# Kernel tuning notes

Measured on AMD Instinct MI355X. Metric: run time of the kernel, lower is better.

Reference implementation:

```python
import jax, jax.numpy as jnp
import numpy as np

D_MODEL = 1024
N_HEADS = 16
D_HEAD = 64
B, S = 2, 2048


def setup_inputs() -> dict:
    key = jax.random.key(0)
    ks = jax.random.split(key, 16)
    HDH = N_HEADS * D_HEAD
    s = 0.02
    return {
        "h": jax.random.normal(ks[0], (B, S, D_MODEL), dtype=jnp.float32),
        "att_mask": jax.random.randint(ks[1], (B, S), 0, 2) > 0,
        "Wq": jax.random.normal(ks[2], (D_MODEL, HDH), dtype=jnp.float32) * s,
        "bq": jnp.zeros((HDH,), dtype=jnp.float32),
        "Wkv": jax.random.normal(ks[3], (D_MODEL, 2 * HDH), dtype=jnp.float32) * s,
        "bkv": jnp.zeros((2 * HDH,), dtype=jnp.float32),
        "Wo": jax.random.normal(ks[4], (HDH, D_MODEL), dtype=jnp.float32) * s,
        "bo": jnp.zeros((D_MODEL,), dtype=jnp.float32),
        "W1": jax.random.normal(ks[5], (D_MODEL, D_MODEL), dtype=jnp.float32) * s,
        "b1": jnp.zeros((D_MODEL,), dtype=jnp.float32),
        "W2": jax.random.normal(ks[6], (D_MODEL, D_MODEL), dtype=jnp.float32) * s,
        "b2": jnp.zeros((D_MODEL,), dtype=jnp.float32),
        "ln_g": jnp.ones((D_MODEL,), dtype=jnp.float32),
        "ln_b": jnp.zeros((D_MODEL,), dtype=jnp.float32),
    }


def _layer_norm(x, g, b, eps=1e-6):
    mu = jnp.mean(x, axis=-1, keepdims=True)
    var = jnp.mean(jnp.square(x - mu), axis=-1, keepdims=True)
    return (x - mu) * jax.lax.rsqrt(var + eps) * g + b


def reference(h, att_mask, Wq, bq, Wkv, bkv, Wo, bo, W1, b1, W2, b2, ln_g, ln_b):
    bz, ln, _ = h.shape
    scale = 1.0 / (D_HEAD ** 0.5)
    q = (h @ Wq + bq).reshape(bz, ln, N_HEADS, D_HEAD)
    kv = h @ Wkv + bkv
    k, v = jnp.split(kv, 2, axis=-1)
    k = k.reshape(bz, ln, N_HEADS, D_HEAD)
    v = v.reshape(bz, ln, N_HEADS, D_HEAD)
    # scores: [b, heads, len_q, len_k]
    scores = jnp.einsum('bqhd,bkhd->bhqk', q, k) * scale
    scores = jnp.where(att_mask[:, None, None, :], -1e9, scores)
    probs = jax.nn.softmax(scores, axis=-1)
    att = jnp.einsum('bhqk,bkhd->bqhd', probs, v).reshape(bz, ln, N_HEADS * D_HEAD)
    att_out = att @ Wo + bo
    # glu_type == 1
    g = jax.nn.sigmoid(h @ W1 + b1) * (h @ W2 + b2)
    return _layer_norm(h + att_out + g, ln_g, ln_b)
```

## Files before the change

kernel.cpp:

```cpp
#include <hip/hip_runtime.h>
#include <hip/hip_bf16.h>


typedef short bf16x8 __attribute__((ext_vector_type(8)));
typedef float f32x4  __attribute__((ext_vector_type(4)));
typedef float f32x16 __attribute__((ext_vector_type(16)));
typedef unsigned int u32x4 __attribute__((ext_vector_type(4)));

typedef const __attribute__((address_space(1))) void* gas_cvp;
typedef __attribute__((address_space(3))) void* las_vp;

__device__ __forceinline__ void gload_lds16(const void* g, void* l) {
  __builtin_amdgcn_global_load_lds((gas_cvp)g, (las_vp)l, 16, 0, 0);
}

__device__ __forceinline__ short f2bf(float f) {
  __hip_bfloat16 h = __float2bfloat16(f);
  return *reinterpret_cast<short*>(&h);
}
__device__ __forceinline__ float bf2f(short s) {
  unsigned u = ((unsigned)(unsigned short)s) << 16;
  return __builtin_bit_cast(float, u);
}

#if __has_builtin(__builtin_amdgcn_exp2f)
#define EXP2(x) __builtin_amdgcn_exp2f(x)
#else
#define EXP2(x) exp2f(x)
#endif

constexpr int BATCH = 2;
constexpr int SEQ   = 2048;
constexpr int NH    = 16;
constexpr int MROWS = BATCH * SEQ;
constexpr int NSPLIT = 2;
constexpr int KSPL   = SEQ / NSPLIT;
constexpr int RH     = MROWS * NH;


__global__ __launch_bounds__(256) void cvt_bf16(const float* __restrict__ src,
                                                short* __restrict__ dst, int n4) {
  int i = blockIdx.x * 256 + threadIdx.x;
  if (i >= n4) return;
  float4 v = reinterpret_cast<const float4*>(src)[i];
  short4 o;
  o.x = f2bf(v.x); o.y = f2bf(v.y); o.z = f2bf(v.z); o.w = f2bf(v.w);
  reinterpret_cast<short4*>(dst)[i] = o;
}

struct WtA {
  const float* s[6];
  short* d[6];
  int st[6];
  int mul[6];
  int add[6];
};
__global__ __launch_bounds__(256) void wtrans6(WtA a) {
  __shared__ float tile[32][33];
  const float* __restrict__ src = a.s[blockIdx.z];
  short* __restrict__ dst = a.d[blockIdx.z];
  const int stride = a.st[blockIdx.z];
  const int mul = a.mul[blockIdx.z], add = a.add[blockIdx.z];
  const int tx = threadIdx.x & 31, ty = threadIdx.x >> 5;
  const int n0 = blockIdx.x * 32, k0 = blockIdx.y * 32;
  #pragma unroll
  for (int i = 0; i < 32; i += 8)
    tile[ty + i][tx] = src[(size_t)(k0 + ty + i) * stride + n0 + tx];
  __syncthreads();
  #pragma unroll
  for (int i = 0; i < 32; i += 8)
    dst[(size_t)((n0 + ty + i) * mul + add) * 1024 + k0 + tx] = f2bf(tile[tx][ty + i]);
}

__global__ __launch_bounds__(256) void vtrans(const short* __restrict__ qkv,
                                              short* __restrict__ vt) {
  __shared__ short tile[32][33];
  const int tx = threadIdx.x & 31, ty = threadIdx.x >> 5;
  const int s0 = blockIdx.x * 32, d0 = blockIdx.y * 32, b = blockIdx.z;
  #pragma unroll
  for (int i = 0; i < 32; i += 8)
    tile[ty + i][tx] = qkv[(size_t)(b * SEQ + s0 + ty + i) * 3072 + 2048 + d0 + tx];
  __syncthreads();
  #pragma unroll
  for (int i = 0; i < 32; i += 8)
    vt[(size_t)(b * 1024 + d0 + ty + i) * SEQ + s0 + tx] = tile[tx][ty + i];
}

__global__ void pack_bias(const float* __restrict__ bq, const float* __restrict__ bkv,
                          const float* __restrict__ b1, const float* __restrict__ b2,
                          float* __restrict__ ball) {
  int i = blockIdx.x * 256 + threadIdx.x;
  if (i < 1024) ball[i] = bq[i];
  else if (i < 3072) ball[i] = bkv[i - 1024];
  else if (i < 4096) {
    const int j = i - 3072;
    ball[3072 + 2 * j] = b1[j];
    ball[3072 + 2 * j + 1] = b2[j];
  }
}

__device__ __forceinline__ bool mask_at(const void* mp, int idx, int flag) {
  if (flag == 1) return ((const int*)mp)[idx] != 0;
  if (flag == 2) return ((const float*)mp)[idx] != 0.f;
  return ((const unsigned char*)mp)[idx] != 0;
}

__global__ __launch_bounds__(256) void premask(const void* __restrict__ msk,
                                               float* __restrict__ mbL) {
  __shared__ int si, sf;
  const unsigned* m = (const unsigned*)msk;
  if (threadIdx.x == 0) { si = 1; sf = 1; }
  __syncthreads();
  bool oki = true, okf = true;
  for (int i = threadIdx.x; i < 1024; i += 256) {
    unsigned v = m[i];
    oki = oki && (v <= 1u);
    okf = okf && (v == 0u || v == 0x3F800000u);
  }
  if (!oki) si = 0;
  if (!okf) sf = 0;
  __syncthreads();
  const int flag = si ? 1 : (sf ? 2 : 0);
  int i = blockIdx.x * 256 + threadIdx.x;
  if (i < MROWS) mbL[i] = mask_at(msk, i, flag) ? -1.442695e9f : -8.0f;
}


template <int BN>
__global__ __launch_bounds__(256) void gemm_bf16(const short* __restrict__ A,
                                                 const short* __restrict__ BT,
                                                 const float* __restrict__ bias,
                                                 short* __restrict__ outp, int N) {
  constexpr int NF = BN / 64;
  __shared__ short Alds[128 * 64];
  __shared__ short Blds[BN * 64];
  const int tid = threadIdx.x;
  const int w = tid >> 6, l = tid & 63, lr = l & 15;
  const int wr = w >> 1, wc = w & 1;
  const int bm = blockIdx.y, bn = blockIdx.x;

  f32x4 acc[4][2 * NF] = {};

  const int srow = tid >> 3;
  const int schunk = (tid & 7) ^ (srow & 7);
  const short* Ab = A  + (size_t)(bm * 128 + srow) * 1024 + schunk * 8;
  const short* Bb = BT + (size_t)(bn * BN + srow) * 1024 + schunk * 8;

  const int cg = (l >> 4) ^ (l & 3), fl = (l >> 2) & 1;
  const short* ard[2] = { &Alds[(wr * 64 + lr) * 64 + cg * 8 + fl * 32],
                          &Alds[(wr * 64 + lr) * 64 + cg * 8 + 32 - fl * 32] };
  const short* brd[2] = { &Blds[(wc * (BN / 2) + lr) * 64 + cg * 8 + fl * 32],
                          &Blds[(wc * (BN / 2) + lr) * 64 + cg * 8 + 32 - fl * 32] };

  for (int kt = 0; kt < 16; ++kt) {
    const int kb = kt * 64;
    __syncthreads();
    #pragma unroll
    for (int q = 0; q < 4; ++q)
      gload_lds16(Ab + (size_t)q * 32 * 1024 + kb, &Alds[q * 2048 + tid * 8]);
    #pragma unroll
    for (int q = 0; q < BN / 32; ++q)
      gload_lds16(Bb + (size_t)q * 32 * 1024 + kb, &Blds[q * 2048 + tid * 8]);
    asm volatile("s_waitcnt vmcnt(0)" ::: "memory");
    __syncthreads();

    #pragma unroll
    for (int s = 0; s < 2; ++s) {
      bf16x8 af[4], bfr[2 * NF];
      #pragma unroll
      for (int m = 0; m < 4; ++m)
        af[m] = *reinterpret_cast<const bf16x8*>(ard[s] + m * 16 * 64);
      #pragma unroll
      for (int n = 0; n < 2 * NF; ++n)
        bfr[n] = *reinterpret_cast<const bf16x8*>(brd[s] + n * 16 * 64);
      #pragma unroll
      for (int m = 0; m < 4; ++m)
        #pragma unroll
        for (int n = 0; n < 2 * NF; ++n)
          acc[m][n] = __builtin_amdgcn_mfma_f32_16x16x32_bf16(af[m], bfr[n], acc[m][n], 0, 0, 0);
    }
  }

  const int g = l >> 4;
  #pragma unroll
  for (int m = 0; m < 4; ++m) {
    const int row = bm * 128 + wr * 64 + m * 16 + g * 4;
    #pragma unroll
    for (int n = 0; n < 2 * NF; ++n) {
      const int col = bn * BN + wc * (BN / 2) + n * 16 + lr;
      const float bv = bias[col];
      #pragma unroll
      for (int r = 0; r < 4; ++r)
        outp[(size_t)(row + r) * N + col] = f2bf(acc[m][n][r] + bv);
    }
  }
}

__global__ __launch_bounds__(256) void gemm_qkvglu(const short* __restrict__ A,
                                                   const short* __restrict__ BT,
                                                   const float* __restrict__ bias,
                                                   short* __restrict__ qkv,
                                                   short* __restrict__ x1) {
  __shared__ short Alds[128 * 64];
  __shared__ short Blds[128 * 64];
  const int tid = threadIdx.x;
  const int w = tid >> 6, l = tid & 63, lr = l & 15;
  const int wr = w >> 1, wc = w & 1;
  const int idx = blockIdx.x;
  const int local = idx >> 3;
  const int bm = (idx & 7) * 4 + (local & 3);
  const int bn = local >> 2;

  f32x4 acc[4][4] = {};

  const int srow = tid >> 3;
  const int schunk = (tid & 7) ^ (srow & 7);
  const short* Ab = A  + (size_t)(bm * 128 + srow) * 1024 + schunk * 8;
  const short* Bb = BT + (size_t)(bn * 128 + srow) * 1024 + schunk * 8;

  const int cg = (l >> 4) ^ (l & 3), fl = (l >> 2) & 1;
  const short* ard[2] = { &Alds[(wr * 64 + lr) * 64 + cg * 8 + fl * 32],
                          &Alds[(wr * 64 + lr) * 64 + cg * 8 + 32 - fl * 32] };
  const short* brd[2] = { &Blds[(wc * 64 + lr) * 64 + cg * 8 + fl * 32],
                          &Blds[(wc * 64 + lr) * 64 + cg * 8 + 32 - fl * 32] };

  for (int kt = 0; kt < 16; ++kt) {
    const int kb = kt * 64;
    __syncthreads();
    #pragma unroll
    for (int q = 0; q < 4; ++q) {
      gload_lds16(Ab + (size_t)q * 32 * 1024 + kb, &Alds[q * 2048 + tid * 8]);
      gload_lds16(Bb + (size_t)q * 32 * 1024 + kb, &Blds[q * 2048 + tid * 8]);
    }
    asm volatile("s_waitcnt vmcnt(0)" ::: "memory");
    __syncthreads();

    #pragma unroll
    for (int s = 0; s < 2; ++s) {
      bf16x8 af[4], bfr[4];
      #pragma unroll
      for (int m = 0; m < 4; ++m)
        af[m] = *reinterpret_cast<const bf16x8*>(ard[s] + m * 16 * 64);
      #pragma unroll
      for (int n = 0; n < 4; ++n)
        bfr[n] = *reinterpret_cast<const bf16x8*>(brd[s] + n * 16 * 64);
      #pragma unroll
      for (int m = 0; m < 4; ++m)
        #pragma unroll
        for (int n = 0; n < 4; ++n)
          acc[m][n] = __builtin_amdgcn_mfma_f32_16x16x32_bf16(af[m], bfr[n], acc[m][n], 0, 0, 0);
    }
  }

  const int g = l >> 4;
  const bool isGlu = (bn >= 24);
  #pragma unroll
  for (int m = 0; m < 4; ++m) {
    const int row = bm * 128 + wr * 64 + m * 16 + g * 4;
    #pragma unroll
    for (int n = 0; n < 4; ++n) {
      const int col = bn * 128 + wc * 64 + n * 16 + lr;
      const float bv = bias[col];
      #pragma unroll
      for (int r = 0; r < 4; ++r) {
        const float v = acc[m][n][r] + bv;
        if (!isGlu) {
          qkv[(size_t)(row + r) * 3072 + col] = f2bf(v);
        } else {
          const float vp = __shfl_xor(v, 1);
          if (!(lr & 1)) {
            const int col2 = col - 3072;
            x1[(size_t)(row + r) * 1024 + (col2 >> 1)] = f2bf(vp / (1.f + __expf(-v)));
          }
        }
      }
    }
  }
}

constexpr int KB = 64;
constexpr int KSLOT = 8 * 66;
constexpr int VSLOT = 8 * 66;

__global__ __launch_bounds__(256) void attn_kernel(const short* __restrict__ qkv,
                                                   const short* __restrict__ vt,
                                                   const float* __restrict__ mbL,
                                                   short* __restrict__ opart,
                                                   float* __restrict__ spart) {
  __shared__ short Kl[2][KSLOT * 8];
  __shared__ short Vl[2][VSLOT * 8];
  __shared__ float mb[KSPL];

  const int tid = threadIdx.x;
  const int w = tid >> 6, lane = tid & 63, ql = lane & 31, hi = lane >> 5;
  const int idx = blockIdx.x;
  const int swz = (idx & 7) * 128 + (idx >> 3);
  const int sp = swz & 1, qb = (swz >> 1) & 15;
  const int h = (swz >> 5) & 15, b = swz >> 9;
  const int qrow = qb * 128 + w * 32 + ql;
  const int kofs = sp * KSPL;

  bf16x8 qf[4];
  {
    const short* qp = qkv + (size_t)(b * SEQ + qrow) * 3072 + h * 64;
    #pragma unroll
    for (int c = 0; c < 4; ++c)
      qf[c] = *reinterpret_cast<const bf16x8*>(qp + c * 16 + hi * 8);
  }

  const short* gkbase = qkv + (size_t)(b * SEQ + kofs) * 3072 + 1024 + h * 64
                        + (size_t)(tid >> 3) * 3072 + (tid & 7) * 8;
  const short* gvbase = vt + ((size_t)(b * 1024 + h * 64) + (tid >> 3)) * SEQ + kofs
                        + (tid & 7) * 8;
  short* kwr = &Kl[0][((tid & 7) * 66 + (tid >> 3)) * 8];
  short* vwr = &Vl[0][((tid & 7) * 66 + (tid >> 3)) * 8];

  u32x4 kreg0, kreg1, vreg0, vreg1;
  auto loadTile = [&](int kt) {
    const short* gk = gkbase + (size_t)kt * KB * 3072;
    kreg0 = *reinterpret_cast<const u32x4*>(gk);
    kreg1 = *reinterpret_cast<const u32x4*>(gk + 32 * 3072);
    const short* gv = gvbase + kt * KB;
    vreg0 = *reinterpret_cast<const u32x4*>(gv);
    vreg1 = *reinterpret_cast<const u32x4*>(gv + 32 * SEQ);
  };
  auto writeTile = [&](int buf) {
    short* kd = kwr + buf * KSLOT * 8;
    *reinterpret_cast<u32x4*>(kd)          = kreg0;
    *reinterpret_cast<u32x4*>(kd + 32 * 8) = kreg1;
    short* vd = vwr + buf * VSLOT * 8;
    *reinterpret_cast<u32x4*>(vd)          = vreg0;
    *reinterpret_cast<u32x4*>(vd + 32 * 8) = vreg1;
  };

  float s_run = 0.f;
  f32x16 oacc0 = {}, oacc1 = {};

  gload_lds16(mbL + b * SEQ + kofs + tid * 4, &mb[tid * 4]);
  loadTile(0);
  writeTile(0);
  __syncthreads();

  const short* krd = &Kl[0][(hi * 66 + ql) * 8];
  const short* vrd = &Vl[0][(hi * 66 + ql) * 8];

  constexpr int NT = KSPL / KB;
  for (int kt = 0; kt < NT; ++kt) {
    const int cur = kt & 1;
    if (kt + 1 < NT) loadTile(kt + 1);
    const short* Kb = krd + cur * KSLOT * 8;
    const short* Vb = vrd + cur * VSLOT * 8;

    #pragma unroll
    for (int t2 = 0; t2 < 2; ++t2) {
      f32x16 sc = {};
      __builtin_amdgcn_s_setprio(1);
      #pragma unroll
      for (int c = 0; c < 4; ++c) {
        bf16x8 kf = *reinterpret_cast<const bf16x8*>(Kb + (c * 132 + t2 * 32) * 8);
        sc = __builtin_amdgcn_mfma_f32_32x32x16_bf16(kf, qf[c], sc, 0, 0, 0);
      }
      __builtin_amdgcn_s_setprio(0);
      float p[16];
      #pragma unroll
      for (int u = 0; u < 4; ++u) {
        float4 m4 = *reinterpret_cast<const float4*>(&mb[kt * KB + t2 * 32 + u * 8 + hi * 4]);
        p[4 * u + 0] = EXP2(fmaf(sc[4 * u + 0], 0.18033688f, m4.x));
        p[4 * u + 1] = EXP2(fmaf(sc[4 * u + 1], 0.18033688f, m4.y));
        p[4 * u + 2] = EXP2(fmaf(sc[4 * u + 2], 0.18033688f, m4.z));
        p[4 * u + 3] = EXP2(fmaf(sc[4 * u + 3], 0.18033688f, m4.w));
      }
      {
        float a0 = (p[0] + p[1]) + (p[2] + p[3]);
        float a1 = (p[4] + p[5]) + (p[6] + p[7]);
        float a2 = (p[8] + p[9]) + (p[10] + p[11]);
        float a3 = (p[12] + p[13]) + (p[14] + p[15]);
        s_run += (a0 + a1) + (a2 + a3);
      }
      unsigned P[8];
      #pragma unroll
      for (int j = 0; j < 8; ++j)
        asm("v_cvt_pk_bf16_f32 %0, %1, %2" : "=v"(P[j]) : "v"(p[2 * j]), "v"(p[2 * j + 1]));
      asm("v_permlane32_swap_b32 %0, %1" : "+v"(P[0]), "+v"(P[2]));
      asm("v_permlane32_swap_b32 %0, %1" : "+v"(P[1]), "+v"(P[3]));
      asm("v_permlane32_swap_b32 %0, %1" : "+v"(P[4]), "+v"(P[6]));
      asm("v_permlane32_swap_b32 %0, %1" : "+v"(P[5]), "+v"(P[7]));
      u32x4 c0 = { P[0], P[1], P[2], P[3] };
      u32x4 c1 = { P[4], P[5], P[6], P[7] };
      bf16x8 pf[2] = { __builtin_bit_cast(bf16x8, c0), __builtin_bit_cast(bf16x8, c1) };

      __builtin_amdgcn_s_setprio(1);
      #pragma unroll
      for (int ch = 0; ch < 2; ++ch) {
        const int gb = (t2 * 4 + ch * 2) * 66;
        bf16x8 v0 = *reinterpret_cast<const bf16x8*>(Vb + gb * 8);
        bf16x8 v1 = *reinterpret_cast<const bf16x8*>(Vb + (gb + 32) * 8);
        oacc0 = __builtin_amdgcn_mfma_f32_32x32x16_bf16(v0, pf[ch], oacc0, 0, 0, 0);
        oacc1 = __builtin_amdgcn_mfma_f32_32x32x16_bf16(v1, pf[ch], oacc1, 0, 0, 0);
      }
      __builtin_amdgcn_s_setprio(0);
    }

    if (kt + 1 < NT) {
      writeTile(cur ^ 1);
      __syncthreads();
    }
  }

  const float sT = s_run + __shfl_xor(s_run, 32);
  const size_t obase = (size_t)sp * RH * 64 + (size_t)(b * SEQ + qrow) * 1024 + h * 64;
  #pragma unroll
  for (int dt = 0; dt < 2; ++dt) {
    #pragma unroll
    for (int u = 0; u < 4; ++u) {
      short4 st;
      const f32x16& oa = dt ? oacc1 : oacc0;
      st.x = f2bf(oa[4 * u + 0]);
      st.y = f2bf(oa[4 * u + 1]);
      st.z = f2bf(oa[4 * u + 2]);
      st.w = f2bf(oa[4 * u + 3]);
      *reinterpret_cast<short4*>(&opart[obase + dt * 32 + u * 8 + hi * 4]) = st;
    }
  }
  if (hi == 0)
    spart[sp * RH + (b * SEQ + qrow) * NH + h] = sT;
}

__global__ __launch_bounds__(256) void attn_merge(const short* __restrict__ opart,
                                                  const float* __restrict__ spart,
                                                  short* __restrict__ att) {
  const int idx = blockIdx.x * 256 + threadIdx.x;
  const int rh = idx >> 3;
  const size_t base = (size_t)rh * 64 + (idx & 7) * 8;
  float acc[8] = {};
  float ss = 0.f;
  #pragma unroll
  for (int s = 0; s < NSPLIT; ++s) {
    bf16x8 o = *reinterpret_cast<const bf16x8*>(&opart[(size_t)s * RH * 64 + base]);
    #pragma unroll
    for (int j = 0; j < 8; ++j) acc[j] += bf2f(o[j]);
    ss += spart[s * RH + rh];
  }
  const float inv = 1.f / ss;
  bf16x8 r;
  #pragma unroll
  for (int j = 0; j < 8; ++j) r[j] = f2bf(acc[j] * inv);
  *reinterpret_cast<bf16x8*>(&att[base]) = r;
}

__global__ __launch_bounds__(256) void ln_kernel(const float* __restrict__ h,
                                                 const short* __restrict__ ao,
                                                 const short* __restrict__ gl,
                                                 const float* __restrict__ gamma,
                                                 const float* __restrict__ beta,
                                                 float* __restrict__ out) {
  const int row = blockIdx.x;
  const size_t base = (size_t)row * 1024;
  const int t = threadIdx.x;
  __shared__ float red[4];
  float4 x = reinterpret_cast<const float4*>(h + base)[t];
  const short4 a4 = reinterpret_cast<const short4*>(ao + base)[t];
  const short4 g4 = reinterpret_cast<const short4*>(gl + base)[t];
  x.x += bf2f(a4.x) + bf2f(g4.x);
  x.y += bf2f(a4.y) + bf2f(g4.y);
  x.z += bf2f(a4.z) + bf2f(g4.z);
  x.w += bf2f(a4.w) + bf2f(g4.w);
  float s = (x.x + x.y) + (x.z + x.w);
  #pragma unroll
  for (int d = 1; d < 64; d <<= 1) s += __shfl_xor(s, d);
  if ((t & 63) == 0) red[t >> 6] = s;
  __syncthreads();
  const float mu = (red[0] + red[1] + red[2] + red[3]) * (1.f / 1024.f);
  __syncthreads();
  const float dx0 = x.x - mu, dx1 = x.y - mu, dx2 = x.z - mu, dx3 = x.w - mu;
  float vs = (dx0 * dx0 + dx1 * dx1) + (dx2 * dx2 + dx3 * dx3);
  #pragma unroll
  for (int d = 1; d < 64; d <<= 1) vs += __shfl_xor(vs, d);
  if ((t & 63) == 0) red[t >> 6] = vs;
  __syncthreads();
  const float var = (red[0] + red[1] + red[2] + red[3]) * (1.f / 1024.f);
  const float rs = rsqrtf(var + 1e-6f);
  const float4 gm = reinterpret_cast<const float4*>(gamma)[t];
  const float4 bt = reinterpret_cast<const float4*>(beta)[t];
  float4 o;
  o.x = dx0 * rs * gm.x + bt.x;
  o.y = dx1 * rs * gm.y + bt.y;
  o.z = dx2 * rs * gm.z + bt.z;
  o.w = dx3 * rs * gm.w + bt.w;
  reinterpret_cast<float4*>(out + base)[t] = o;
}


extern "C" void kernel_launch(void* const* d_in, const int* in_sizes, int n_in,
                              void* d_out, int out_size, void* d_ws, size_t ws_size,
                              hipStream_t stream) {
  const float* h   = (const float*)d_in[0];
  const void*  msk = d_in[1];
  const float* Wq  = (const float*)d_in[2];
  const float* bq  = (const float*)d_in[3];
  const float* Wkv = (const float*)d_in[4];
  const float* bkv = (const float*)d_in[5];
  const float* Wo  = (const float*)d_in[6];
  const float* bo  = (const float*)d_in[7];
  const float* W1  = (const float*)d_in[8];
  const float* b1  = (const float*)d_in[9];
  const float* W2  = (const float*)d_in[10];
  const float* b2  = (const float*)d_in[11];
  const float* lng = (const float*)d_in[12];
  const float* lnb = (const float*)d_in[13];
  float* out = (float*)d_out;

  char* ws = (char*)d_ws;
  size_t off = 0;
  auto alloc = [&](size_t bytes) {
    char* p = ws + off;
    off += (bytes + 255) & ~(size_t)255;
    return p;
  };
  short* X     = (short*)alloc((size_t)MROWS * 1024 * 2);
  short* WALL  = (short*)alloc((size_t)5120 * 1024 * 2);
  short* WoT   = (short*)alloc((size_t)1024 * 1024 * 2);
  float* ball  = (float*)alloc(5120 * 4);
  float* MBL   = (float*)alloc((size_t)MROWS * 4);
  short* QKV   = (short*)alloc((size_t)MROWS * 3072 * 2);
  short* VT    = (short*)alloc((size_t)BATCH * 1024 * SEQ * 2);
  short* ATT   = (short*)alloc((size_t)MROWS * 1024 * 2);
  short* X1    = (short*)alloc((size_t)MROWS * 1024 * 2);
  short* AO    = (short*)alloc((size_t)MROWS * 1024 * 2);
  short* OP    = (short*)alloc((size_t)NSPLIT * RH * 64 * 2);
  float* SP    = (float*)alloc((size_t)NSPLIT * RH * 4);
  if (off > ws_size) return;

  cvt_bf16<<<4096, 256, 0, stream>>>(h, X, MROWS * 1024 / 4);
  WtA wa;
  wa.s[0] = Wq;          wa.d[0] = WALL;                wa.st[0] = 1024;  wa.mul[0] = 1; wa.add[0] = 0;
  wa.s[1] = Wkv;         wa.d[1] = WALL + 1024 * 1024;  wa.st[1] = 2048;  wa.mul[1] = 1; wa.add[1] = 0;
  wa.s[2] = Wkv + 1024;  wa.d[2] = WALL + 2048 * 1024;  wa.st[2] = 2048;  wa.mul[2] = 1; wa.add[2] = 0;
  wa.s[3] = Wo;          wa.d[3] = WoT;                 wa.st[3] = 1024;  wa.mul[3] = 1; wa.add[3] = 0;
  wa.s[4] = W1;          wa.d[4] = WALL + 3072 * 1024;  wa.st[4] = 1024;  wa.mul[4] = 2; wa.add[4] = 0;
  wa.s[5] = W2;          wa.d[5] = WALL + 3072 * 1024;  wa.st[5] = 1024;  wa.mul[5] = 2; wa.add[5] = 1;
  wtrans6<<<dim3(32, 32, 6), 256, 0, stream>>>(wa);
  pack_bias<<<16, 256, 0, stream>>>(bq, bkv, b1, b2, ball);
  premask<<<16, 256, 0, stream>>>(msk, MBL);

  gemm_qkvglu<<<1280, 256, 0, stream>>>(X, WALL, ball, QKV, X1);
  vtrans<<<dim3(64, 32, 2), 256, 0, stream>>>(QKV, VT);
  attn_kernel<<<1024, 256, 0, stream>>>(QKV, VT, MBL, OP, SP);
  attn_merge<<<RH * 8 / 256, 256, 0, stream>>>(OP, SP, ATT);
  gemm_bf16<64><<<dim3(16, 32), 256, 0, stream>>>(ATT, WoT, bo, AO, 1024);
  ln_kernel<<<MROWS, 256, 0, stream>>>(h, AO, X1, lng, lnb, out);
}
```

Baseline: 166.4 us.

## Fuse V transpose into QKV GEMM epilogue and drop attention split-K merge

The QKV/GLU GEMM epilogue now writes the V columns directly in transposed layout, which removes the separate vtrans kernel. Attention no longer splits the key range in two. Each block processes the full sequence and normalises its output in place, which removes the attn_merge kernel and the partial-output buffers. The trade-off is half as many attention blocks (512 instead of 1024), so each block runs a longer serial loop and occupancy on the device is lower. The transposed V stores are also strided short4 writes.

```diff
diff --git a/kernel.cpp b/kernel.cpp
--- a/kernel.cpp
+++ b/kernel.cpp
@@ -33,9 +33,6 @@
 constexpr int SEQ   = 2048;
 constexpr int NH    = 16;
 constexpr int MROWS = BATCH * SEQ;
-constexpr int NSPLIT = 2;
-constexpr int KSPL   = SEQ / NSPLIT;
-constexpr int RH     = MROWS * NH;
 
 
 __global__ __launch_bounds__(256) void cvt_bf16(const float* __restrict__ src,
@@ -72,20 +69,6 @@
     dst[(size_t)((n0 + ty + i) * mul + add) * 1024 + k0 + tx] = f2bf(tile[tx][ty + i]);
 }
 
-__global__ __launch_bounds__(256) void vtrans(const short* __restrict__ qkv,
-                                              short* __restrict__ vt) {
-  __shared__ short tile[32][33];
-  const int tx = threadIdx.x & 31, ty = threadIdx.x >> 5;
-  const int s0 = blockIdx.x * 32, d0 = blockIdx.y * 32, b = blockIdx.z;
-  #pragma unroll
-  for (int i = 0; i < 32; i += 8)
-    tile[ty + i][tx] = qkv[(size_t)(b * SEQ + s0 + ty + i) * 3072 + 2048 + d0 + tx];
-  __syncthreads();
-  #pragma unroll
-  for (int i = 0; i < 32; i += 8)
-    vt[(size_t)(b * 1024 + d0 + ty + i) * SEQ + s0 + tx] = tile[tx][ty + i];
-}
-
 __global__ void pack_bias(const float* __restrict__ bq, const float* __restrict__ bkv,
                           const float* __restrict__ b1, const float* __restrict__ b2,
                           float* __restrict__ ball) {
@@ -200,6 +183,7 @@
                                                    const short* __restrict__ BT,
                                                    const float* __restrict__ bias,
                                                    short* __restrict__ qkv,
+                                                   short* __restrict__ vt,
                                                    short* __restrict__ x1) {
   __shared__ short Alds[128 * 64];
   __shared__ short Blds[128 * 64];
@@ -253,7 +237,6 @@
   }
 
   const int g = l >> 4;
-  const bool isGlu = (bn >= 24);
   #pragma unroll
   for (int m = 0; m < 4; ++m) {
     const int row = bm * 128 + wr * 64 + m * 16 + g * 4;
@@ -261,18 +244,26 @@
     for (int n = 0; n < 4; ++n) {
       const int col = bn * 128 + wc * 64 + n * 16 + lr;
       const float bv = bias[col];
-      #pragma unroll
-      for (int r = 0; r < 4; ++r) {
-        const float v = acc[m][n][r] + bv;
-        if (!isGlu) {
-          qkv[(size_t)(row + r) * 3072 + col] = f2bf(v);
-        } else {
-          const float vp = __shfl_xor(v, 1);
-          if (!(lr & 1)) {
-            const int col2 = col - 3072;
-            x1[(size_t)(row + r) * 1024 + (col2 >> 1)] = f2bf(vp / (1.f + __expf(-v)));
-          }
+      float v[4];
+      #pragma unroll
+      for (int r = 0; r < 4; ++r) v[r] = acc[m][n][r] + bv;
+      if (bn >= 24) {
+        #pragma unroll
+        for (int r = 0; r < 4; ++r) {
+          const float vp = __shfl_xor(v[r], 1);
+          if (!(lr & 1))
+            x1[(size_t)(row + r) * 1024 + ((col - 3072) >> 1)] =
+                f2bf(vp / (1.f + __expf(-v[r])));
         }
+      } else if (col < 2048) {
+        #pragma unroll
+        for (int r = 0; r < 4; ++r)
+          qkv[(size_t)(row + r) * 3072 + col] = f2bf(v[r]);
+      } else {
+        short4 st;
+        st.x = f2bf(v[0]); st.y = f2bf(v[1]); st.z = f2bf(v[2]); st.w = f2bf(v[3]);
+        *reinterpret_cast<short4*>(
+            &vt[((size_t)((row >> 11) * 1024 + (col - 2048))) * SEQ + (row & 2047)]) = st;
       }
     }
   }
@@ -285,20 +276,17 @@
 __global__ __launch_bounds__(256) void attn_kernel(const short* __restrict__ qkv,
                                                    const short* __restrict__ vt,
                                                    const float* __restrict__ mbL,
-                                                   short* __restrict__ opart,
-                                                   float* __restrict__ spart) {
+                                                   short* __restrict__ att) {
   __shared__ short Kl[2][KSLOT * 8];
   __shared__ short Vl[2][VSLOT * 8];
-  __shared__ float mb[KSPL];
+  __shared__ float mb[SEQ];
 
   const int tid = threadIdx.x;
   const int w = tid >> 6, lane = tid & 63, ql = lane & 31, hi = lane >> 5;
   const int idx = blockIdx.x;
-  const int swz = (idx & 7) * 128 + (idx >> 3);
-  const int sp = swz & 1, qb = (swz >> 1) & 15;
-  const int h = (swz >> 5) & 15, b = swz >> 9;
+  const int swz = (idx & 7) * 64 + (idx >> 3);
+  const int qb = swz & 15, h = (swz >> 4) & 15, b = swz >> 8;
   const int qrow = qb * 128 + w * 32 + ql;
-  const int kofs = sp * KSPL;
 
   bf16x8 qf[4];
   {
@@ -308,9 +296,9 @@
       qf[c] = *reinterpret_cast<const bf16x8*>(qp + c * 16 + hi * 8);
   }
 
-  const short* gkbase = qkv + (size_t)(b * SEQ + kofs) * 3072 + 1024 + h * 64
+  const short* gkbase = qkv + (size_t)(b * SEQ) * 3072 + 1024 + h * 64
                         + (size_t)(tid >> 3) * 3072 + (tid & 7) * 8;
-  const short* gvbase = vt + ((size_t)(b * 1024 + h * 64) + (tid >> 3)) * SEQ + kofs
+  const short* gvbase = vt + ((size_t)(b * 1024 + h * 64) + (tid >> 3)) * SEQ
                         + (tid & 7) * 8;
   short* kwr = &Kl[0][((tid & 7) * 66 + (tid >> 3)) * 8];
   short* vwr = &Vl[0][((tid & 7) * 66 + (tid >> 3)) * 8];
@@ -336,7 +324,8 @@
   float s_run = 0.f;
   f32x16 oacc0 = {}, oacc1 = {};
 
-  gload_lds16(mbL + b * SEQ + kofs + tid * 4, &mb[tid * 4]);
+  gload_lds16(mbL + b * SEQ + tid * 4, &mb[tid * 4]);
+  gload_lds16(mbL + b * SEQ + 1024 + tid * 4, &mb[1024 + tid * 4]);
   loadTile(0);
   writeTile(0);
   __syncthreads();
@@ -344,7 +333,7 @@
   const short* krd = &Kl[0][(hi * 66 + ql) * 8];
   const short* vrd = &Vl[0][(hi * 66 + ql) * 8];
 
-  constexpr int NT = KSPL / KB;
+  constexpr int NT = SEQ / KB;
   for (int kt = 0; kt < NT; ++kt) {
     const int cur = kt & 1;
     if (kt + 1 < NT) loadTile(kt + 1);
@@ -408,44 +397,21 @@
   }
 
   const float sT = s_run + __shfl_xor(s_run, 32);
-  const size_t obase = (size_t)sp * RH * 64 + (size_t)(b * SEQ + qrow) * 1024 + h * 64;
+  const float inv = 1.f / sT;
+  const size_t obase = (size_t)(b * SEQ + qrow) * 1024 + h * 64;
   #pragma unroll
   for (int dt = 0; dt < 2; ++dt) {
     #pragma unroll
     for (int u = 0; u < 4; ++u) {
       short4 st;
       const f32x16& oa = dt ? oacc1 : oacc0;
-      st.x = f2bf(oa[4 * u + 0]);
-      st.y = f2bf(oa[4 * u + 1]);
-      st.z = f2bf(oa[4 * u + 2]);
-      st.w = f2bf(oa[4 * u + 3]);
-      *reinterpret_cast<short4*>(&opart[obase + dt * 32 + u * 8 + hi * 4]) = st;
-    }
-  }
-  if (hi == 0)
-    spart[sp * RH + (b * SEQ + qrow) * NH + h] = sT;
-}
-
-__global__ __launch_bounds__(256) void attn_merge(const short* __restrict__ opart,
-                                                  const float* __restrict__ spart,
-                                                  short* __restrict__ att) {
-  const int idx = blockIdx.x * 256 + threadIdx.x;
-  const int rh = idx >> 3;
-  const size_t base = (size_t)rh * 64 + (idx & 7) * 8;
-  float acc[8] = {};
-  float ss = 0.f;
-  #pragma unroll
-  for (int s = 0; s < NSPLIT; ++s) {
-    bf16x8 o = *reinterpret_cast<const bf16x8*>(&opart[(size_t)s * RH * 64 + base]);
-    #pragma unroll
-    for (int j = 0; j < 8; ++j) acc[j] += bf2f(o[j]);
-    ss += spart[s * RH + rh];
-  }
-  const float inv = 1.f / ss;
-  bf16x8 r;
-  #pragma unroll
-  for (int j = 0; j < 8; ++j) r[j] = f2bf(acc[j] * inv);
-  *reinterpret_cast<bf16x8*>(&att[base]) = r;
+      st.x = f2bf(oa[4 * u + 0] * inv);
+      st.y = f2bf(oa[4 * u + 1] * inv);
+      st.z = f2bf(oa[4 * u + 2] * inv);
+      st.w = f2bf(oa[4 * u + 3] * inv);
+      *reinterpret_cast<short4*>(&att[obase + dt * 32 + u * 8 + hi * 4]) = st;
+    }
+  }
 }
 
 __global__ __launch_bounds__(256) void ln_kernel(const float* __restrict__ h,
@@ -527,8 +493,6 @@
   short* ATT   = (short*)alloc((size_t)MROWS * 1024 * 2);
   short* X1    = (short*)alloc((size_t)MROWS * 1024 * 2);
   short* AO    = (short*)alloc((size_t)MROWS * 1024 * 2);
-  short* OP    = (short*)alloc((size_t)NSPLIT * RH * 64 * 2);
-  float* SP    = (float*)alloc((size_t)NSPLIT * RH * 4);
   if (off > ws_size) return;
 
   cvt_bf16<<<4096, 256, 0, stream>>>(h, X, MROWS * 1024 / 4);
@@ -543,10 +507,8 @@
   pack_bias<<<16, 256, 0, stream>>>(bq, bkv, b1, b2, ball);
   premask<<<16, 256, 0, stream>>>(msk, MBL);
 
-  gemm_qkvglu<<<1280, 256, 0, stream>>>(X, WALL, ball, QKV, X1);
-  vtrans<<<dim3(64, 32, 2), 256, 0, stream>>>(QKV, VT);
-  attn_kernel<<<1024, 256, 0, stream>>>(QKV, VT, MBL, OP, SP);
-  attn_merge<<<RH * 8 / 256, 256, 0, stream>>>(OP, SP, ATT);
+  gemm_qkvglu<<<1280, 256, 0, stream>>>(X, WALL, ball, QKV, VT, X1);
+  attn_kernel<<<512, 256, 0, stream>>>(QKV, VT, MBL, ATT);
   gemm_bf16<64><<<dim3(16, 32), 256, 0, stream>>>(ATT, WoT, bo, AO, 1024);
   ln_kernel<<<MROWS, 256, 0, stream>>>(h, AO, X1, lng, lnb, out);
 }
```

After: 158.2 us (median of 2 runs). 1.05x faster.
